# Performance work log

Measured on AMD Instinct MI355X. Metric: run time of the kernel, lower is better.

## Reference

```python
import jax, jax.numpy as jnp
import numpy as np

N = 100000   # nodes
E = 1600000  # edges (self-loop free by construction)
B = 512      # graphs in batch
F = 128      # input node features
HID = 128    # hidden dim
HEADS = 4
CH = HID // HEADS  # 32
EPS_BN = 1e-5


def setup_inputs() -> dict:
    key = jax.random.key(0)
    ks = jax.random.split(key, 24)
    x = jax.random.normal(ks[0], (N, F), jnp.float32)
    dst = jax.random.randint(ks[1], (E,), 0, N)
    off = jax.random.randint(ks[2], (E,), 1, N)
    src = (dst + off) % N  # guaranteed no self loops
    edge_index = jnp.stack([src, dst]).astype(jnp.int32)
    batch = jnp.sort(jax.random.randint(ks[3], (N,), 0, B)).astype(jnp.int32)
    g = lambda k, shape, fan: jax.random.normal(k, shape, jnp.float32) / np.sqrt(fan)
    return {
        "x": x, "edge_index": edge_index, "batch": batch,
        "W_in": g(ks[4], (F, HID), F), "b_in": jnp.zeros((HID,), jnp.float32),
        "lin_w": g(ks[5], (2, HID, HID), HID),
        "att_src": g(ks[6], (2, HEADS, CH), CH),
        "att_dst": g(ks[7], (2, HEADS, CH), CH),
        "conv_b": jnp.zeros((2, HID), jnp.float32),
        "lin_w_last": g(ks[8], (HID, HID), HID),
        "att_src_last": g(ks[9], (HID,), HID),
        "att_dst_last": g(ks[10], (HID,), HID),
        "b_last": jnp.zeros((HID,), jnp.float32),
        "bn_g": jnp.ones((3, HID), jnp.float32) + 0.1 * jax.random.normal(ks[11], (3, HID), jnp.float32),
        "bn_b": 0.1 * jax.random.normal(ks[12], (3, HID), jnp.float32),
        "bn_m": 0.1 * jax.random.normal(ks[13], (3, HID), jnp.float32),
        "bn_v": 0.5 + jax.random.uniform(ks[14], (3, HID), jnp.float32),
        "ro_w1": g(ks[15], (HID, HID // 2), HID),
        "ro_b1": jnp.zeros((HID // 2,), jnp.float32),
        "ro_w2": g(ks[16], (HID // 2, 1), HID // 2),
        "ro_b2": jnp.zeros((1,), jnp.float32),
    }


def _gat_conv(h, src, dst, W, a_src, a_dst, bias, concat):
    """PyG GATConv (shared lin for src/dst, add_self_loops=True, eval mode)."""
    n = h.shape[0]
    heads, ch = a_src.shape
    xs = (h @ W).reshape(n, heads, ch)              # [N,H,C]
    al_s = jnp.sum(xs * a_src, axis=-1)             # [N,H]
    al_d = jnp.sum(xs * a_dst, axis=-1)             # [N,H]
    loop = jnp.arange(n, dtype=src.dtype)
    src_f = jnp.concatenate([src, loop])
    dst_f = jnp.concatenate([dst, loop])
    e = jax.nn.leaky_relu(al_s[src_f] + al_d[dst_f], 0.2)   # [E+N,H]
    m = jax.ops.segment_max(e, dst_f, num_segments=n)       # dest-grouped softmax
    ee = jnp.exp(e - m[dst_f])
    z = jax.ops.segment_sum(ee, dst_f, num_segments=n)
    alpha = ee / (z[dst_f] + 1e-16)                          # [E+N,H]
    out = jax.ops.segment_sum(alpha[:, :, None] * xs[src_f], dst_f, num_segments=n)
    out = out.reshape(n, heads * ch) if concat else jnp.mean(out, axis=1)
    return out + bias


def _bn_eval(h, g, b, m, v):
    return (h - m) * (g / jnp.sqrt(v + EPS_BN)) + b


def _seg_softmax(scores, seg, num_segments):
    m = jax.ops.segment_max(scores, seg, num_segments=num_segments)
    e = jnp.exp(scores - m[seg])
    z = jax.ops.segment_sum(e, seg, num_segments=num_segments)
    return e / z[seg]


def reference(x, edge_index, batch, W_in, b_in, lin_w, att_src, att_dst, conv_b,
              lin_w_last, att_src_last, att_dst_last, b_last,
              bn_g, bn_b, bn_m, bn_v, ro_w1, ro_b1, ro_w2, ro_b2):
    src, dst = edge_index[0], edge_index[1]
    h = x @ W_in + b_in                                       # input_proj
    # first num_layers-1 multi-head concat layers
    for i in range(2):
        h_new = _gat_conv(h, src, dst, lin_w[i], att_src[i], att_dst[i], conv_b[i], True)
        h_new = jax.nn.elu(_bn_eval(h_new, bn_g[i], bn_b[i], bn_m[i], bn_v[i]))
        h = h + h_new                                         # residual (shapes match)
    # final single-head layer, concat=False
    h_new = _gat_conv(h, src, dst, lin_w_last, att_src_last[None, :], att_dst_last[None, :], b_last, False)
    h_new = jax.nn.elu(_bn_eval(h_new, bn_g[2], bn_b[2], bn_m[2], bn_v[2]))
    h = h + h_new
    # attention readout + per-graph softmax over atoms
    atom_scores = (jnp.tanh(h @ ro_w1 + ro_b1) @ ro_w2 + ro_b2)[:, 0]   # [N]
    atom_attention = _seg_softmax(atom_scores, batch, B)
    # attention-weighted add pool
    graph_emb = jax.ops.segment_sum(h * atom_attention[:, None], batch, num_segments=B)
    return graph_emb, atom_attention
```

## Files before the change

kernel.cpp:

```cpp
#include <hip/hip_runtime.h>
#include <math.h>
#include <stdint.h>

#define BSZ 512
#define BSH 9
#define NBKT_MAX 256

typedef __attribute__((ext_vector_type(8))) short bf16x8;
typedef __attribute__((ext_vector_type(4))) float f32x4;

static __device__ __forceinline__ uint32_t f2bf(float x) {
    uint32_t u = __float_as_uint(x);
    return (u + 0x7fffu + ((u >> 16) & 1u)) >> 16;
}
static __device__ __forceinline__ float bflo(uint32_t v) { return __uint_as_float(v << 16); }
static __device__ __forceinline__ float bfhi(uint32_t v) { return __uint_as_float(v & 0xffff0000u); }
static __device__ __forceinline__ void split2(float x, short& hi, short& lo) {
    uint32_t hb = f2bf(x);
    float hf = __uint_as_float(hb << 16);
    uint32_t lb = f2bf(x - hf);
    hi = (short)hb; lo = (short)lb;
}

__global__ void k_binit(int* __restrict__ bcur, int nbkt, int cap) {
    int t = threadIdx.x;
    if (t < nbkt) bcur[t] = t * cap;
}
__global__ __launch_bounds__(256) void k_bucket(const int* __restrict__ src, const int* __restrict__ dst,
                                                int* __restrict__ bcur, uint32_t* __restrict__ bucketed,
                                                int e, int cap) {
    __shared__ int hist[NBKT_MAX];
    __shared__ int cur[NBKT_MAX];
    int t = threadIdx.x;
    hist[t] = 0;
    __syncthreads();
    int base = blockIdx.x * 8192;
#pragma unroll 4
    for (int i = 0; i < 32; ++i) {
        int ei = base + i * 256 + t;
        if (ei < e) atomicAdd(&hist[dst[ei] >> BSH], 1);
    }
    __syncthreads();
    int hc = hist[t];
    cur[t] = (hc > 0) ? atomicAdd(&bcur[t], hc) : 0;
    __syncthreads();
#pragma unroll 4
    for (int i = 0; i < 32; ++i) {
        int ei = base + i * 256 + t;
        if (ei < e) {
            int d = dst[ei], s = src[ei];
            int b = d >> BSH;
            int p = atomicAdd(&cur[b], 1);
            if (p < (b + 1) * cap)
                bucketed[p] = ((uint32_t)(d & (BSZ - 1)) << 23) | (uint32_t)s;
        }
    }
}
__global__ __launch_bounds__(256) void k_bcount(const int* __restrict__ bcur, const uint32_t* __restrict__ bucketed,
                                                int* __restrict__ cnt, int n, int cap) {
    __shared__ int lf[BSZ];
    int b = blockIdx.x, t = threadIdx.x;
    int n0 = b << BSH;
    int nn = min(BSZ, n - n0);
    for (int i = t; i < nn; i += 256) lf[i] = 0;
    __syncthreads();
    int cb = min(bcur[b] - b * cap, cap);
    const uint32_t* ba = bucketed + (size_t)b * cap;
    for (int i = t; i < cb; i += 256) atomicAdd(&lf[ba[i] >> 23], 1);
    __syncthreads();
    for (int i = t; i < nn; i += 256) cnt[n0 + i] = lf[i] + 1;
}
__global__ __launch_bounds__(256) void k_scan1(const int* __restrict__ cnt, int* __restrict__ bsum, int n) {
    __shared__ int sd[256];
    int base = blockIdx.x * 1024, t = threadIdx.x;
    int s = 0;
#pragma unroll
    for (int i = 0; i < 4; ++i) {
        int idx = base + t * 4 + i;
        if (idx < n) s += (cnt[idx] + 3) & ~3;
    }
    sd[t] = s; __syncthreads();
    for (int o = 128; o; o >>= 1) {
        if (t < o) sd[t] += sd[t + o];
        __syncthreads();
    }
    if (t == 0) bsum[blockIdx.x] = sd[0];
}
__global__ void k_scan2(int* __restrict__ bsum, int nb) {
    __shared__ int sd[128];
    int t = threadIdx.x;
    int v = (t < nb) ? bsum[t] : 0;
    sd[t] = v; __syncthreads();
    for (int o = 1; o < 128; o <<= 1) {
        int u = (t >= o) ? sd[t - o] : 0;
        __syncthreads();
        sd[t] += u;
        __syncthreads();
    }
    if (t < nb) bsum[t] = sd[t] - v;
}
__global__ __launch_bounds__(256) void k_scan3(const int* __restrict__ cnt, const int* __restrict__ bsum,
                                               int* __restrict__ rp, int n) {
    __shared__ int sd[256];
    int base = blockIdx.x * 1024, t = threadIdx.x;
    int v[4]; int s = 0;
#pragma unroll
    for (int i = 0; i < 4; ++i) {
        int idx = base + t * 4 + i;
        v[i] = (idx < n) ? ((cnt[idx] + 3) & ~3) : 0;
        s += v[i];
    }
    sd[t] = s; __syncthreads();
    for (int o = 1; o < 256; o <<= 1) {
        int u = (t >= o) ? sd[t - o] : 0;
        __syncthreads();
        sd[t] += u;
        __syncthreads();
    }
    int excl = sd[t] - s + bsum[blockIdx.x];
#pragma unroll
    for (int i = 0; i < 4; ++i) {
        int idx = base + t * 4 + i;
        if (idx < n) rp[idx] = excl;
        excl += v[i];
        if (idx == n - 1) rp[n] = excl;
    }
}
__global__ __launch_bounds__(256) void k_bscatter(const int* __restrict__ bcur, const uint32_t* __restrict__ bucketed,
                                                  const int* __restrict__ rp, int* __restrict__ col,
                                                  int n, int cap) {
    __shared__ int lf[BSZ];
    __shared__ int rpl[BSZ];
    int b = blockIdx.x, t = threadIdx.x;
    int n0 = b << BSH;
    int nn = min(BSZ, n - n0);
    for (int i = t; i < nn; i += 256) {
        int r = rp[n0 + i];
        rpl[i] = r;
        lf[i] = 1;
        col[r] = n0 + i;
    }
    __syncthreads();
    int cb = min(bcur[b] - b * cap, cap);
    const uint32_t* ba = bucketed + (size_t)b * cap;
    for (int i = t; i < cb; i += 256) {
        uint32_t v = ba[i];
        int ld = (int)(v >> 23), s = (int)(v & 0x7fffffu);
        int o = atomicAdd(&lf[ld], 1);
        col[rpl[ld] + o] = s;
    }
    __syncthreads();
    for (int i = t; i < nn; i += 256) {
        int c = lf[i], end = (c + 3) & ~3;
        int r = rpl[i];
        for (int j = c; j < end; ++j) col[r + j] = -1;
    }
}
__global__ void k_bnprep(const float* __restrict__ conv_b, const float* __restrict__ b_last,
                         const float* __restrict__ bn_g, const float* __restrict__ bn_b,
                         const float* __restrict__ bn_m, const float* __restrict__ bn_v,
                         float* __restrict__ sc, float* __restrict__ sh) {
    int i = blockIdx.x * 128 + threadIdx.x;
    if (i >= 384) return;
    int layer = i >> 7, c = i & 127;
    float bias = (layer < 2) ? conv_b[layer * 128 + c] : b_last[c];
    float s = bn_g[i] * __frsqrt_rn(bn_v[i] + 1e-5f);
    sc[i] = s;
    sh[i] = (bias - bn_m[i]) * s + bn_b[i];
}
__global__ __launch_bounds__(256) void k_wprep(const float* __restrict__ W_in, const float* __restrict__ lin_w,
                                               const float* __restrict__ lin_w_last,
                                               uint16_t* __restrict__ wfh, uint16_t* __restrict__ wfl) {
    int i = blockIdx.x * 256 + threadIdx.x;
    int m = i >> 14, e = i & 16383;
    const float* src = (m == 0) ? W_in : (m == 1) ? lin_w : (m == 2) ? (lin_w + 16384) : lin_w_last;
    float v = src[e];
    int k = e >> 7, n = e & 127;
    int kc = k >> 5, g = (k >> 3) & 3, j = k & 7, ct = n >> 4, cln = n & 15;
    int idx = m * 16384 + (((kc * 8 + ct) * 64) + g * 16 + cln) * 8 + j;
    short hi, lo;
    split2(v, hi, lo);
    wfh[idx] = hi; wfl[idx] = lo;
}

template <int ATT, int OBF>
__global__ __launch_bounds__(256) void k_gemm(
    const float* __restrict__ A, const uint16_t* __restrict__ wfh, const uint16_t* __restrict__ wfl,
    const float* __restrict__ bias, void* __restrict__ outv,
    const float* __restrict__ atts, const float* __restrict__ attd,
    float* __restrict__ als, float* __restrict__ ald, int nrows)
{
    __shared__ __align__(16) char smem[4 * 16 * 132 * 4];
    const int t = threadIdx.x;
    const int l = t & 63, wv = t >> 6;
    const int cl = l & 15, gl = l >> 4;
    const int row0w = blockIdx.x * 128 + wv * 32;

    float bloc[8], avsl[8], avdl[8];
    if (ATT == 0) {
#pragma unroll
        for (int ct = 0; ct < 8; ++ct) bloc[ct] = bias[ct * 16 + cl];
    } else {
#pragma unroll
        for (int ct = 0; ct < 8; ++ct) { avsl[ct] = atts[ct * 16 + cl]; avdl[ct] = attd[ct * 16 + cl]; }
    }

    bf16x8 Ah[2][4], Al[2][4];
#pragma unroll
    for (int rt = 0; rt < 2; ++rt) {
        int row = row0w + rt * 16 + cl;
        bool ok = row < nrows;
        const float* ap = A + (size_t)row * 128 + gl * 8;
#pragma unroll
        for (int kc = 0; kc < 4; ++kc) {
            float4 u = make_float4(0.f, 0.f, 0.f, 0.f), v = u;
            if (ok) {
                u = *(const float4*)(ap + kc * 32);
                v = *(const float4*)(ap + kc * 32 + 4);
            }
            float xv[8] = {u.x, u.y, u.z, u.w, v.x, v.y, v.z, v.w};
            bf16x8 hbv, lbv;
#pragma unroll
            for (int j = 0; j < 8; ++j) {
                short hi, lo;
                split2(xv[j], hi, lo);
                hbv[j] = hi; lbv[j] = lo;
            }
            Ah[rt][kc] = hbv; Al[rt][kc] = lbv;
        }
    }

    f32x4 acc[2][8];
#pragma unroll
    for (int rt = 0; rt < 2; ++rt)
#pragma unroll
        for (int ct = 0; ct < 8; ++ct) { f32x4 z = {0.f, 0.f, 0.f, 0.f}; acc[rt][ct] = z; }
#pragma unroll
    for (int kc = 0; kc < 4; ++kc) {
        bf16x8 bh[8], bl[8];
#pragma unroll
        for (int ct = 0; ct < 8; ++ct) {
            bh[ct] = *(const bf16x8*)(wfh + (size_t)(((kc * 8 + ct) * 64) + l) * 8);
            bl[ct] = *(const bf16x8*)(wfl + (size_t)(((kc * 8 + ct) * 64) + l) * 8);
        }
#pragma unroll
        for (int rt = 0; rt < 2; ++rt)
#pragma unroll
            for (int ct = 0; ct < 8; ++ct) {
                acc[rt][ct] = __builtin_amdgcn_mfma_f32_16x16x32_bf16(Ah[rt][kc], bh[ct], acc[rt][ct], 0, 0, 0);
                acc[rt][ct] = __builtin_amdgcn_mfma_f32_16x16x32_bf16(Ah[rt][kc], bl[ct], acc[rt][ct], 0, 0, 0);
                acc[rt][ct] = __builtin_amdgcn_mfma_f32_16x16x32_bf16(Al[rt][kc], bh[ct], acc[rt][ct], 0, 0, 0);
            }
    }

    if (OBF) {
        uint16_t* out = (uint16_t*)outv;
        uint16_t* buf = (uint16_t*)smem + wv * (16 * 144);
#pragma unroll
        for (int rt = 0; rt < 2; ++rt) {
#pragma unroll
            for (int ct = 0; ct < 8; ++ct)
#pragma unroll
                for (int r = 0; r < 4; ++r)
                    buf[(gl * 4 + r) * 144 + ct * 16 + cl] = (uint16_t)f2bf(acc[rt][ct][r]);
#pragma unroll
            for (int ri = 0; ri < 4; ++ri) {
                int rloc = ri * 4 + gl;
                int row = row0w + rt * 16 + rloc;
                if (row < nrows) {
                    uint4 v = *(const uint4*)&buf[rloc * 144 + cl * 8];
                    *(uint4*)&out[(size_t)row * 128 + cl * 8] = v;
                }
            }
        }
    } else {
        float* out = (float*)outv;
        float* buf = (float*)smem + wv * (16 * 132);
#pragma unroll
        for (int rt = 0; rt < 2; ++rt) {
#pragma unroll
            for (int ct = 0; ct < 8; ++ct)
#pragma unroll
                for (int r = 0; r < 4; ++r)
                    buf[(gl * 4 + r) * 132 + ct * 16 + cl] = acc[rt][ct][r] + bloc[ct];
#pragma unroll
            for (int ri = 0; ri < 4; ++ri) {
                int rloc = ri * 4 + gl;
                int row = row0w + rt * 16 + rloc;
                if (row < nrows) {
                    float4 v0 = *(const float4*)&buf[rloc * 132 + cl * 8];
                    float4 v1 = *(const float4*)&buf[rloc * 132 + cl * 8 + 4];
                    *(float4*)&out[(size_t)row * 128 + cl * 8] = v0;
                    *(float4*)&out[(size_t)row * 128 + cl * 8 + 4] = v1;
                }
            }
        }
    }

    if (ATT == 4) {
#pragma unroll
        for (int rt = 0; rt < 2; ++rt)
#pragma unroll
            for (int r = 0; r < 4; ++r) {
                float s[4], d[4];
#pragma unroll
                for (int hh = 0; hh < 4; ++hh) {
                    s[hh] = acc[rt][2 * hh][r] * avsl[2 * hh] + acc[rt][2 * hh + 1][r] * avsl[2 * hh + 1];
                    d[hh] = acc[rt][2 * hh][r] * avdl[2 * hh] + acc[rt][2 * hh + 1][r] * avdl[2 * hh + 1];
                }
#pragma unroll
                for (int hh = 0; hh < 4; ++hh) {
                    s[hh] += __shfl_xor(s[hh], 1); s[hh] += __shfl_xor(s[hh], 2);
                    s[hh] += __shfl_xor(s[hh], 4); s[hh] += __shfl_xor(s[hh], 8);
                    d[hh] += __shfl_xor(d[hh], 1); d[hh] += __shfl_xor(d[hh], 2);
                    d[hh] += __shfl_xor(d[hh], 4); d[hh] += __shfl_xor(d[hh], 8);
                }
                int row = row0w + rt * 16 + gl * 4 + r;
                if (row < nrows && cl < 4) { als[row * 4 + cl] = s[cl]; ald[row * 4 + cl] = d[cl]; }
            }
    } else if (ATT == 1) {
#pragma unroll
        for (int rt = 0; rt < 2; ++rt)
#pragma unroll
            for (int r = 0; r < 4; ++r) {
                float s = 0.f, d = 0.f;
#pragma unroll
                for (int ct = 0; ct < 8; ++ct) {
                    s += acc[rt][ct][r] * avsl[ct];
                    d += acc[rt][ct][r] * avdl[ct];
                }
                s += __shfl_xor(s, 1); s += __shfl_xor(s, 2); s += __shfl_xor(s, 4); s += __shfl_xor(s, 8);
                d += __shfl_xor(d, 1); d += __shfl_xor(d, 2); d += __shfl_xor(d, 4); d += __shfl_xor(d, 8);
                int row = row0w + rt * 16 + gl * 4 + r;
                if (row < nrows && cl == 0) { als[row] = s; ald[row] = d; }
            }
    }
}

#define BC4(q) __int_as_float(__builtin_amdgcn_ds_swizzle(pi, 0x10 | ((q) << 5)))
#define GATH(i, u) uint32_t x##i = *(const uint32_t*)(xsb + ((size_t)(u) << 7));
#define EDGE8_H4(Q) do { \
    int4 ca = *(const int4*)&col[j + (Q)]; \
    int4 cb = *(const int4*)&col[j + (Q) + 4]; \
    float p0 = BC4((Q)+0), p1 = BC4((Q)+1), p2 = BC4((Q)+2), p3 = BC4((Q)+3); \
    float p4 = BC4((Q)+4), p5 = BC4((Q)+5), p6 = BC4((Q)+6), p7 = BC4((Q)+7); \
    int u0 = max(ca.x, 0), u1 = max(ca.y, 0), u2 = max(ca.z, 0), u3 = max(ca.w, 0); \
    int u4 = max(cb.x, 0), u5 = max(cb.y, 0), u6 = max(cb.z, 0), u7 = max(cb.w, 0); \
    GATH(0, u0) GATH(1, u1) GATH(2, u2) GATH(3, u3) \
    GATH(4, u4) GATH(5, u5) GATH(6, u6) GATH(7, u7) \
    a0 = fmaf(p0, bflo(x0), fmaf(p1, bflo(x1), fmaf(p2, bflo(x2), fmaf(p3, bflo(x3), a0)))); \
    a0 = fmaf(p4, bflo(x4), fmaf(p5, bflo(x5), fmaf(p6, bflo(x6), fmaf(p7, bflo(x7), a0)))); \
    a1 = fmaf(p0, bfhi(x0), fmaf(p1, bfhi(x1), fmaf(p2, bfhi(x2), fmaf(p3, bfhi(x3), a1)))); \
    a1 = fmaf(p4, bfhi(x4), fmaf(p5, bfhi(x5), fmaf(p6, bfhi(x6), fmaf(p7, bfhi(x7), a1)))); \
} while (0)
#define EDGE4_H4(Q) do { \
    int4 ca = *(const int4*)&col[j + (Q)]; \
    float p0 = BC4((Q)+0), p1 = BC4((Q)+1), p2 = BC4((Q)+2), p3 = BC4((Q)+3); \
    int u0 = max(ca.x, 0), u1 = max(ca.y, 0), u2 = max(ca.z, 0), u3 = max(ca.w, 0); \
    GATH(0, u0) GATH(1, u1) GATH(2, u2) GATH(3, u3) \
    a0 = fmaf(p0, bflo(x0), fmaf(p1, bflo(x1), fmaf(p2, bflo(x2), fmaf(p3, bflo(x3), a0)))); \
    a1 = fmaf(p0, bfhi(x0), fmaf(p1, bfhi(x1), fmaf(p2, bfhi(x2), fmaf(p3, bfhi(x3), a1)))); \
} while (0)

template <int H>
__global__ __launch_bounds__(256) void k_agg(
    const int* __restrict__ rp, const int* __restrict__ col,
    const float* __restrict__ als, const float* __restrict__ ald_,
    const uint16_t* __restrict__ xs, const float* __restrict__ bnsc,
    const float* __restrict__ bnsh, float* __restrict__ h, int n)
{
    constexpr int EPG = (H == 4) ? 16 : 64;
    int node = blockIdx.x * 4 + (threadIdx.x >> 6);
    if (node >= n) return;
    int l = threadIdx.x & 63;
    int hl = (H == 4) ? (l >> 4) : 0;
    int c0 = l * 2;
    float ad = ald_[node * H + hl];
    int jb = rp[node], je = rp[node + 1];
    float2 hv = *(const float2*)&h[(size_t)node * 128 + c0];
    float sc0v = bnsc[c0], sc1v = bnsc[c0 + 1];
    float sh0v = bnsh[c0], sh1v = bnsh[c0 + 1];
    const uint16_t* xsb = xs + c0;

    float zl = 0.f, a0 = 0.f, a1 = 0.f;
    for (int j = jb; j < je; j += EPG) {
        int e_l = j + (l & (EPG - 1));
        int s_l = (e_l < je) ? col[e_l] : -1;
        int t_l = max(s_l, 0);
        float lg = ((H == 4) ? als[t_l * 4 + hl] : als[t_l]) + ad;
        lg = fmaxf(lg, 0.2f * lg);
        float p_l = (s_l < 0) ? 0.f : __expf(lg);
        zl += p_l;
        int pi = __float_as_int(p_l);
        int ng = min(EPG, je - j);
        if (H == 4) {
            if (ng == 16)      { EDGE8_H4(0); EDGE8_H4(8); }
            else if (ng == 12) { EDGE8_H4(0); EDGE4_H4(8); }
            else if (ng == 8)  { EDGE8_H4(0); }
            else               { EDGE4_H4(0); }
        } else {
            int q = 0;
            for (; q + 8 <= ng; q += 8) {
                int4 ca = *(const int4*)&col[j + q];
                int4 cb = *(const int4*)&col[j + q + 4];
                float p0 = __shfl(p_l, q + 0), p1 = __shfl(p_l, q + 1);
                float p2 = __shfl(p_l, q + 2), p3 = __shfl(p_l, q + 3);
                float p4 = __shfl(p_l, q + 4), p5 = __shfl(p_l, q + 5);
                float p6 = __shfl(p_l, q + 6), p7 = __shfl(p_l, q + 7);
                int u0 = max(ca.x, 0), u1 = max(ca.y, 0), u2 = max(ca.z, 0), u3 = max(ca.w, 0);
                int u4 = max(cb.x, 0), u5 = max(cb.y, 0), u6 = max(cb.z, 0), u7 = max(cb.w, 0);
                GATH(0, u0) GATH(1, u1) GATH(2, u2) GATH(3, u3)
                GATH(4, u4) GATH(5, u5) GATH(6, u6) GATH(7, u7)
                a0 = fmaf(p0, bflo(x0), fmaf(p1, bflo(x1), fmaf(p2, bflo(x2), fmaf(p3, bflo(x3), a0))));
                a0 = fmaf(p4, bflo(x4), fmaf(p5, bflo(x5), fmaf(p6, bflo(x6), fmaf(p7, bflo(x7), a0))));
                a1 = fmaf(p0, bfhi(x0), fmaf(p1, bfhi(x1), fmaf(p2, bfhi(x2), fmaf(p3, bfhi(x3), a1))));
                a1 = fmaf(p4, bfhi(x4), fmaf(p5, bfhi(x5), fmaf(p6, bfhi(x6), fmaf(p7, bfhi(x7), a1))));
            }
            if (q < ng) {
                int4 ca = *(const int4*)&col[j + q];
                float p0 = __shfl(p_l, q + 0), p1 = __shfl(p_l, q + 1);
                float p2 = __shfl(p_l, q + 2), p3 = __shfl(p_l, q + 3);
                int u0 = max(ca.x, 0), u1 = max(ca.y, 0), u2 = max(ca.z, 0), u3 = max(ca.w, 0);
                GATH(0, u0) GATH(1, u1) GATH(2, u2) GATH(3, u3)
                a0 = fmaf(p0, bflo(x0), fmaf(p1, bflo(x1), fmaf(p2, bflo(x2), fmaf(p3, bflo(x3), a0))));
                a1 = fmaf(p0, bfhi(x0), fmaf(p1, bfhi(x1), fmaf(p2, bfhi(x2), fmaf(p3, bfhi(x3), a1))));
            }
        }
    }
    zl += __shfl_xor(zl, 1); zl += __shfl_xor(zl, 2);
    zl += __shfl_xor(zl, 4); zl += __shfl_xor(zl, 8);
    if (H == 1) {
        zl += __shfl_xor(zl, 16); zl += __shfl_xor(zl, 32);
    }
    float inv = 1.f / zl;
    float y0 = fmaf(a0 * inv, sc0v, sh0v);
    float y1 = fmaf(a1 * inv, sc1v, sh1v);
    y0 = y0 > 0.f ? y0 : expm1f(y0);
    y1 = y1 > 0.f ? y1 : expm1f(y1);
    hv.x += y0; hv.y += y1;
    *(float2*)&h[(size_t)node * 128 + c0] = hv;
}

__global__ __launch_bounds__(256) void k_scores(
    const float* __restrict__ h, const float* __restrict__ w1, const float* __restrict__ b1,
    const float* __restrict__ w2, const float* __restrict__ b2,
    float* __restrict__ scores, int n)
{
    __shared__ float W1s[128 * 64];
    __shared__ float As[16][132];
    __shared__ float red[4][32][4];
    const int t = threadIdx.x;
    {
        const float4* w4 = (const float4*)w1;
        float4* s4 = (float4*)W1s;
#pragma unroll
        for (int i = 0; i < 8; ++i) s4[t + i * 256] = w4[t + i * 256];
    }
    const int rg = t & 31, cg = t >> 5;
    const int r0 = rg * 4, c0 = cg * 8;
    const int row0 = blockIdx.x * 128;
    const int ar = (t * 2) >> 2;
    const int ak0 = ((t * 2) & 3) * 4, ak1 = ((t * 2 + 1) & 3) * 4;
    float bloc[8], w2loc[8];
#pragma unroll
    for (int j = 0; j < 8; ++j) { bloc[j] = b1[c0 + j]; w2loc[j] = w2[c0 + j]; }

    float acc[4][8] = {};
    for (int kc = 0; kc < 8; ++kc) {
        __syncthreads();
        {
            float4 v0 = make_float4(0.f, 0.f, 0.f, 0.f), v1 = v0;
            int row = row0 + ar;
            if (row < n) {
                v0 = *(const float4*)&h[(size_t)row * 128 + kc * 16 + ak0];
                v1 = *(const float4*)&h[(size_t)row * 128 + kc * 16 + ak1];
            }
            As[ak0 + 0][ar] = v0.x; As[ak0 + 1][ar] = v0.y; As[ak0 + 2][ar] = v0.z; As[ak0 + 3][ar] = v0.w;
            As[ak1 + 0][ar] = v1.x; As[ak1 + 1][ar] = v1.y; As[ak1 + 2][ar] = v1.z; As[ak1 + 3][ar] = v1.w;
        }
        __syncthreads();
#pragma unroll
        for (int kk = 0; kk < 16; ++kk) {
            float a[4], w[8];
            *(float4*)&a[0] = *(const float4*)&As[kk][r0];
            *(float4*)&w[0] = *(const float4*)&W1s[(kc * 16 + kk) * 64 + c0];
            *(float4*)&w[4] = *(const float4*)&W1s[(kc * 16 + kk) * 64 + c0 + 4];
#pragma unroll
            for (int r = 0; r < 4; ++r)
#pragma unroll
                for (int j = 0; j < 8; ++j) acc[r][j] += a[r] * w[j];
        }
    }
    float part[4];
#pragma unroll
    for (int r = 0; r < 4; ++r) {
        float s = 0.f;
#pragma unroll
        for (int j = 0; j < 8; ++j) s += tanhf(acc[r][j] + bloc[j]) * w2loc[j];
        part[r] = s;
    }
#pragma unroll
    for (int r = 0; r < 4; ++r) part[r] += __shfl_xor(part[r], 32);
    const int wv = t >> 6;
    if ((t & 32) == 0) {
#pragma unroll
        for (int r = 0; r < 4; ++r) red[wv][rg][r] = part[r];
    }
    __syncthreads();
    if (t < 128) {
        int row = row0 + t;
        if (row < n) {
            float s = red[0][t >> 2][t & 3] + red[1][t >> 2][t & 3]
                    + red[2][t >> 2][t & 3] + red[3][t >> 2][t & 3];
            scores[row] = s + b2[0];
        }
    }
}
__global__ void k_graph_ptr(const int* __restrict__ batch, int* __restrict__ gptr, int n, int B) {
    int i = blockIdx.x * 256 + threadIdx.x;
    if (i >= n) return;
    int b = batch[i];
    int bp = (i == 0) ? -1 : batch[i - 1];
    for (int g = bp + 1; g <= b; ++g) gptr[g] = i;
    if (i == n - 1)
        for (int g = b + 1; g <= B; ++g) gptr[g] = n;
}
__global__ __launch_bounds__(256) void k_graph_mz(const int* __restrict__ gptr, const float* __restrict__ scores,
                                                  float* __restrict__ gmax, float* __restrict__ gz, int B) {
    int g = blockIdx.x * 4 + (threadIdx.x >> 6);
    if (g >= B) return;
    int l = threadIdx.x & 63;
    int s0 = gptr[g], s1 = gptr[g + 1];
    float m = -INFINITY;
    for (int i = s0 + l; i < s1; i += 64) m = fmaxf(m, scores[i]);
#pragma unroll
    for (int off = 32; off; off >>= 1) m = fmaxf(m, __shfl_xor(m, off));
    float z = 0.f;
    for (int i = s0 + l; i < s1; i += 64) z += __expf(scores[i] - m);
#pragma unroll
    for (int off = 32; off; off >>= 1) z += __shfl_xor(z, off);
    if (l == 0) { gmax[g] = m; gz[g] = z; }
}
__global__ void k_att(const int* __restrict__ batch, const float* __restrict__ scores,
                      const float* __restrict__ gmax, const float* __restrict__ gz,
                      float* __restrict__ att, int n) {
    int i = blockIdx.x * 256 + threadIdx.x;
    if (i >= n) return;
    int b = batch[i];
    att[i] = __expf(scores[i] - gmax[b]) / gz[b];
}
__global__ __launch_bounds__(256) void k_emb(const int* __restrict__ gptr, const float* __restrict__ att,
                                             const float* __restrict__ h, float* __restrict__ emb) {
    __shared__ float sd[16][64];
    int g = blockIdx.x >> 1, half = blockIdx.x & 1;
    int t = threadIdx.x;
    int cq = (t & 15) * 4;
    int c = half * 64 + cq;
    int p = t >> 4;
    int s0 = gptr[g], s1 = gptr[g + 1];
    float4 acc = make_float4(0.f, 0.f, 0.f, 0.f);
    for (int i = s0 + p; i < s1; i += 16) {
        float a = att[i];
        float4 hvv = *(const float4*)&h[(size_t)i * 128 + c];
        acc.x += a * hvv.x; acc.y += a * hvv.y; acc.z += a * hvv.z; acc.w += a * hvv.w;
    }
    *(float4*)&sd[p][cq] = acc;
    __syncthreads();
    if (t < 64) {
        float s = 0.f;
#pragma unroll
        for (int q = 0; q < 16; ++q) s += sd[q][t];
        emb[g * 128 + half * 64 + t] = s;
    }
}

extern "C" void kernel_launch(void* const* d_in, const int* in_sizes, int n_in,
                              void* d_out, int out_size, void* d_ws, size_t ws_size,
                              hipStream_t stream)
{
    const float* x            = (const float*)d_in[0];
    const int*   eidx         = (const int*)d_in[1];
    const int*   batch        = (const int*)d_in[2];
    const float* W_in         = (const float*)d_in[3];
    const float* b_in         = (const float*)d_in[4];
    const float* lin_w        = (const float*)d_in[5];
    const float* att_src      = (const float*)d_in[6];
    const float* att_dst      = (const float*)d_in[7];
    const float* conv_b       = (const float*)d_in[8];
    const float* lin_w_last   = (const float*)d_in[9];
    const float* att_src_last = (const float*)d_in[10];
    const float* att_dst_last = (const float*)d_in[11];
    const float* b_last       = (const float*)d_in[12];
    const float* bn_g         = (const float*)d_in[13];
    const float* bn_b         = (const float*)d_in[14];
    const float* bn_m         = (const float*)d_in[15];
    const float* bn_v         = (const float*)d_in[16];
    const float* ro_w1        = (const float*)d_in[17];
    const float* ro_b1        = (const float*)d_in[18];
    const float* ro_w2        = (const float*)d_in[19];
    const float* ro_b2        = (const float*)d_in[20];

    const int N = in_sizes[0] / 128;
    const int E = in_sizes[1] / 2;
    const int B = 512;
    const int* esrc = eidx;
    const int* edst = eidx + E;
    const int colcap = E + 4 * N + 64;
    const int NBKT = (N + BSZ - 1) >> BSH;
    const int cap = (E / NBKT) * 3 / 2 + 512;

    char* wsp = (char*)d_ws;
    size_t off = 0;
    auto alloc = [&](size_t bytes) -> void* {
        void* p = wsp + off;
        off += (bytes + 511) & ~(size_t)511;
        return p;
    };
    float*    h      = (float*)alloc((size_t)N * 128 * 4);
    uint16_t* xs     = (uint16_t*)alloc((size_t)N * 128 * 2);
    float*    als    = (float*)alloc((size_t)N * 4 * 4);
    float*    ald    = (float*)alloc((size_t)N * 4 * 4);
    float*    scores = (float*)alloc((size_t)N * 4);
    int*      rp     = (int*)alloc((size_t)(N + 1) * 4);
    int*      col    = (int*)alloc((size_t)colcap * 4);
    int*      cnt    = (int*)alloc((size_t)N * 4);
    int*      bsum   = (int*)alloc(4096);
    int*      gptr   = (int*)alloc((size_t)(B + 1) * 4);
    float*    gmax   = (float*)alloc((size_t)B * 4);
    float*    gz     = (float*)alloc((size_t)B * 4);
    float*    bnsc   = (float*)alloc(384 * 4);
    float*    bnsh   = (float*)alloc(384 * 4);
    int*      bcur   = (int*)alloc(NBKT_MAX * 4);
    uint16_t* wfh    = (uint16_t*)alloc(4 * 16384 * 2);
    uint16_t* wfl    = (uint16_t*)alloc(4 * 16384 * 2);
    uint32_t* bucketed = (uint32_t*)alloc((size_t)NBKT * cap * 4);
    (void)ws_size; (void)n_in; (void)out_size;

    float* emb = (float*)d_out;
    float* att = (float*)d_out + (size_t)B * 128;

    const int nb = (N + 1023) / 1024;
    hipLaunchKernelGGL(k_binit, dim3(1), dim3(256), 0, stream, bcur, NBKT, cap);
    hipLaunchKernelGGL(k_bucket, dim3((E + 8191) / 8192), dim3(256), 0, stream,
                       esrc, edst, bcur, bucketed, E, cap);
    hipLaunchKernelGGL(k_bcount, dim3(NBKT), dim3(256), 0, stream, bcur, bucketed, cnt, N, cap);
    hipLaunchKernelGGL(k_scan1, dim3(nb), dim3(256), 0, stream, cnt, bsum, N);
    hipLaunchKernelGGL(k_scan2, dim3(1), dim3(128), 0, stream, bsum, nb);
    hipLaunchKernelGGL(k_scan3, dim3(nb), dim3(256), 0, stream, cnt, bsum, rp, N);
    hipLaunchKernelGGL(k_bscatter, dim3(NBKT), dim3(256), 0, stream, bcur, bucketed, rp, col, N, cap);
    hipLaunchKernelGGL(k_bnprep, dim3(3), dim3(128), 0, stream, conv_b, b_last, bn_g, bn_b, bn_m, bn_v, bnsc, bnsh);
    hipLaunchKernelGGL(k_wprep, dim3(256), dim3(256), 0, stream, W_in, lin_w, lin_w_last, wfh, wfl);

    const int ntiles = (N + 127) / 128;
    hipLaunchKernelGGL((k_gemm<0, 0>), dim3(ntiles), dim3(256), 0, stream,
                       x, wfh, wfl, b_in, (void*)h, (const float*)nullptr, (const float*)nullptr,
                       (float*)nullptr, (float*)nullptr, N);
    for (int i = 0; i < 2; ++i) {
        hipLaunchKernelGGL((k_gemm<4, 1>), dim3(ntiles), dim3(256), 0, stream,
                           h, wfh + (size_t)(i + 1) * 16384, wfl + (size_t)(i + 1) * 16384,
                           (const float*)nullptr, (void*)xs,
                           att_src + i * 128, att_dst + i * 128, als, ald, N);
        hipLaunchKernelGGL((k_agg<4>), dim3((N + 3) / 4), dim3(256), 0, stream,
                           rp, col, als, ald, xs, bnsc + i * 128, bnsh + i * 128, h, N);
    }
    hipLaunchKernelGGL((k_gemm<1, 1>), dim3(ntiles), dim3(256), 0, stream,
                       h, wfh + (size_t)3 * 16384, wfl + (size_t)3 * 16384,
                       (const float*)nullptr, (void*)xs,
                       att_src_last, att_dst_last, als, ald, N);
    hipLaunchKernelGGL((k_agg<1>), dim3((N + 3) / 4), dim3(256), 0, stream,
                       rp, col, als, ald, xs, bnsc + 256, bnsh + 256, h, N);

    hipLaunchKernelGGL(k_scores, dim3(ntiles), dim3(256), 0, stream,
                       h, ro_w1, ro_b1, ro_w2, ro_b2, scores, N);
    hipLaunchKernelGGL(k_graph_ptr, dim3((N + 255) / 256), dim3(256), 0, stream, batch, gptr, N, B);
    hipLaunchKernelGGL(k_graph_mz, dim3((B + 3) / 4), dim3(256), 0, stream, gptr, scores, gmax, gz, B);
    hipLaunchKernelGGL(k_att, dim3((N + 255) / 256), dim3(256), 0, stream, batch, scores, gmax, gz, att, N);
    hipLaunchKernelGGL(k_emb, dim3(B * 2), dim3(256), 0, stream, gptr, att, h, emb);
}
```

Baseline: 501.7 us.

## Two-pass bucketing of edges by source then destination before CSR build

Replaces the single dst-bucketing pass with a two-level scheme. Edges are first bucketed by source block, then a per-bucket histogram and column scan compute offsets, and a second scatter places edges into dst buckets in src-sorted order. The aim is to make the CSR column lists locality-ordered by source, so the later gather of neighbour features during aggregation hits cache better. In exchange it adds three kernels, an extra edge buffer and an extra full pass over the edges.

```diff
diff --git a/kernel.cpp b/kernel.cpp
--- a/kernel.cpp
+++ b/kernel.cpp
@@ -22,13 +22,13 @@
     hi = (short)hb; lo = (short)lb;
 }
 
-__global__ void k_binit(int* __restrict__ bcur, int nbkt, int cap) {
+__global__ void k_binit(int* __restrict__ bcur2, int nbkt, int cap2) {
     int t = threadIdx.x;
-    if (t < nbkt) bcur[t] = t * cap;
-}
-__global__ __launch_bounds__(256) void k_bucket(const int* __restrict__ src, const int* __restrict__ dst,
-                                                int* __restrict__ bcur, uint32_t* __restrict__ bucketed,
-                                                int e, int cap) {
+    if (t < nbkt) bcur2[t] = t * cap2;
+}
+__global__ __launch_bounds__(256) void k_bucket_src(const int* __restrict__ src, const int* __restrict__ dst,
+                                                    int* __restrict__ bcur2, uint32_t* __restrict__ b2,
+                                                    int e, int cap2) {
     __shared__ int hist[NBKT_MAX];
     __shared__ int cur[NBKT_MAX];
     int t = threadIdx.x;
@@ -38,22 +38,67 @@
 #pragma unroll 4
     for (int i = 0; i < 32; ++i) {
         int ei = base + i * 256 + t;
-        if (ei < e) atomicAdd(&hist[dst[ei] >> BSH], 1);
+        if (ei < e) atomicAdd(&hist[src[ei] >> BSH], 1);
     }
     __syncthreads();
     int hc = hist[t];
-    cur[t] = (hc > 0) ? atomicAdd(&bcur[t], hc) : 0;
+    cur[t] = (hc > 0) ? atomicAdd(&bcur2[t], hc) : 0;
     __syncthreads();
 #pragma unroll 4
     for (int i = 0; i < 32; ++i) {
         int ei = base + i * 256 + t;
         if (ei < e) {
-            int d = dst[ei], s = src[ei];
-            int b = d >> BSH;
+            int s = src[ei], d = dst[ei];
+            int b = s >> BSH;
             int p = atomicAdd(&cur[b], 1);
-            if (p < (b + 1) * cap)
-                bucketed[p] = ((uint32_t)(d & (BSZ - 1)) << 23) | (uint32_t)s;
-        }
+            if (p < (b + 1) * cap2)
+                b2[p] = ((uint32_t)d << 9) | (uint32_t)(s & (BSZ - 1));
+        }
+    }
+}
+__global__ __launch_bounds__(256) void k_hist2(const int* __restrict__ bcur2, const uint32_t* __restrict__ b2,
+                                               int* __restrict__ H, int cap2, int nb) {
+    __shared__ int hist[NBKT_MAX];
+    int j = blockIdx.x, t = threadIdx.x;
+    hist[t] = 0;
+    __syncthreads();
+    int cb = min(bcur2[j] - j * cap2, cap2);
+    const uint32_t* ba = b2 + (size_t)j * cap2;
+    for (int i = t; i < cb; i += 256) atomicAdd(&hist[ba[i] >> (9 + BSH)], 1);
+    __syncthreads();
+    if (t < nb) H[j * nb + t] = hist[t];
+}
+__global__ __launch_bounds__(256) void k_cscan(const int* __restrict__ H, int* __restrict__ HO,
+                                               int* __restrict__ bcur, int cap, int nsb, int nb) {
+    __shared__ int sd[256];
+    int b = blockIdx.x, t = threadIdx.x;
+    int v = (t < nsb) ? H[t * nb + b] : 0;
+    sd[t] = v; __syncthreads();
+    for (int o = 1; o < 256; o <<= 1) {
+        int u = (t >= o) ? sd[t - o] : 0;
+        __syncthreads();
+        sd[t] += u;
+        __syncthreads();
+    }
+    if (t < nsb) HO[t * nb + b] = b * cap + sd[t] - v;
+    if (t == 255) bcur[b] = b * cap + sd[255];
+}
+__global__ __launch_bounds__(256) void k_scatter2(const int* __restrict__ bcur2, const uint32_t* __restrict__ b2,
+                                                  const int* __restrict__ HO, uint32_t* __restrict__ bucketed,
+                                                  int cap2, int nb) {
+    __shared__ int cur[NBKT_MAX];
+    int j = blockIdx.x, t = threadIdx.x;
+    if (t < nb) cur[t] = HO[j * nb + t];
+    __syncthreads();
+    int cb = min(bcur2[j] - j * cap2, cap2);
+    const uint32_t* ba = b2 + (size_t)j * cap2;
+    int s9 = j << BSH;
+    for (int i = t; i < cb; i += 256) {
+        uint32_t v = ba[i];
+        int d = (int)(v >> 9);
+        int s = s9 | (int)(v & (BSZ - 1));
+        int p = atomicAdd(&cur[d >> BSH], 1);
+        bucketed[p] = ((uint32_t)(d & (BSZ - 1)) << 23) | (uint32_t)s;
     }
 }
 __global__ __launch_bounds__(256) void k_bcount(const int* __restrict__ bcur, const uint32_t* __restrict__ bucketed,
@@ -631,18 +676,25 @@
     float*    bnsc   = (float*)alloc(384 * 4);
     float*    bnsh   = (float*)alloc(384 * 4);
     int*      bcur   = (int*)alloc(NBKT_MAX * 4);
+    int*      bcur2  = (int*)alloc(NBKT_MAX * 4);
+    int*      Hm     = (int*)alloc((size_t)NBKT * NBKT * 4);
+    int*      HO     = (int*)alloc((size_t)NBKT * NBKT * 4);
     uint16_t* wfh    = (uint16_t*)alloc(4 * 16384 * 2);
     uint16_t* wfl    = (uint16_t*)alloc(4 * 16384 * 2);
-    uint32_t* bucketed = (uint32_t*)alloc((size_t)NBKT * cap * 4);
+    uint32_t* bucketed  = (uint32_t*)alloc((size_t)NBKT * cap * 4);
+    uint32_t* bucketed2 = (uint32_t*)alloc((size_t)NBKT * cap * 4);
     (void)ws_size; (void)n_in; (void)out_size;
 
     float* emb = (float*)d_out;
     float* att = (float*)d_out + (size_t)B * 128;
 
     const int nb = (N + 1023) / 1024;
-    hipLaunchKernelGGL(k_binit, dim3(1), dim3(256), 0, stream, bcur, NBKT, cap);
-    hipLaunchKernelGGL(k_bucket, dim3((E + 8191) / 8192), dim3(256), 0, stream,
-                       esrc, edst, bcur, bucketed, E, cap);
+    hipLaunchKernelGGL(k_binit, dim3(1), dim3(256), 0, stream, bcur2, NBKT, cap);
+    hipLaunchKernelGGL(k_bucket_src, dim3((E + 8191) / 8192), dim3(256), 0, stream,
+                       esrc, edst, bcur2, bucketed2, E, cap);
+    hipLaunchKernelGGL(k_hist2, dim3(NBKT), dim3(256), 0, stream, bcur2, bucketed2, Hm, cap, NBKT);
+    hipLaunchKernelGGL(k_cscan, dim3(NBKT), dim3(256), 0, stream, Hm, HO, bcur, cap, NBKT, NBKT);
+    hipLaunchKernelGGL(k_scatter2, dim3(NBKT), dim3(256), 0, stream, bcur2, bucketed2, HO, bucketed, cap, NBKT);
     hipLaunchKernelGGL(k_bcount, dim3(NBKT), dim3(256), 0, stream, bcur, bucketed, cnt, N, cap);
     hipLaunchKernelGGL(k_scan1, dim3(nb), dim3(256), 0, stream, cnt, bsum, N);
     hipLaunchKernelGGL(k_scan2, dim3(1), dim3(128), 0, stream, bsum, nb);
```

After: 528.4 us. 5.3% more time.
